# Optimization experiments

Measured on AMD Instinct MI355X. Metric: run time of the kernel, lower is better.

Reference implementation:

```python
import jax, jax.numpy as jnp
import numpy as np

SEQ, D_IN, D_OUT = 4096, 1024, 1024


def setup_inputs() -> dict:
    key = jax.random.key(0)
    k_emb, k_q, k_k, k_v = jax.random.split(key, 4)
    # torch Linear stores weight as [out, in]; we keep [in, out] for x @ W
    scale = 1.0 / np.sqrt(D_IN)
    return {
        "embeddings": jax.random.normal(k_emb, (SEQ, D_IN), dtype=jnp.float32),
        "w_query": jax.random.uniform(k_q, (D_IN, D_OUT), dtype=jnp.float32, minval=-scale, maxval=scale),
        "w_key": jax.random.uniform(k_k, (D_IN, D_OUT), dtype=jnp.float32, minval=-scale, maxval=scale),
        "w_value": jax.random.uniform(k_v, (D_IN, D_OUT), dtype=jnp.float32, minval=-scale, maxval=scale),
    }


def reference(embeddings, w_query, w_key, w_value):
    # QKV projections (bias=False)
    q = embeddings @ w_query  # [S, D_out]
    k = embeddings @ w_key    # [S, D_out]
    v = embeddings @ w_value  # [S, D_out]
    inv_sqrt_d = 1.0 / jnp.sqrt(jnp.asarray(k.shape[-1], dtype=q.dtype))
    scores = jnp.einsum("sd,td->st", q, k) * inv_sqrt_d  # [S, S]
    weights = jax.nn.softmax(scores, axis=-1)
    return weights @ v  # [S, D_out]
```

## Files before the change

kernel.cpp:

```cpp
#include <hip/hip_runtime.h>
#include <hip/hip_bf16.h>

typedef unsigned short u16;
typedef __bf16 bf16x8 __attribute__((ext_vector_type(8)));
typedef float f32x4 __attribute__((ext_vector_type(4)));
typedef unsigned short u16x8 __attribute__((ext_vector_type(8)));
typedef unsigned short u16x4 __attribute__((ext_vector_type(4)));

__device__ __forceinline__ float bf2f(u16 u) {
  unsigned x = ((unsigned)u) << 16;
  return __builtin_bit_cast(float, x);
}
__device__ __forceinline__ u16 f2bf(float f) {
  unsigned u = __builtin_bit_cast(unsigned, f);
  u += 0x7fffu + ((u >> 16) & 1u);
  return (u16)(u >> 16);
}

__device__ __forceinline__ void gload16(const u16* g, u16* lds) {
  __builtin_amdgcn_global_load_lds(
      (const __attribute__((address_space(1))) void*)g,
      (__attribute__((address_space(3))) void*)lds,
      16, 0, 0);
}

__device__ __forceinline__ void bar() {
  __builtin_amdgcn_sched_barrier(0);
  __builtin_amdgcn_s_barrier();
  __builtin_amdgcn_sched_barrier(0);
}
template <int N> __device__ __forceinline__ void wait_vm() {
  asm volatile("s_waitcnt vmcnt(%0)" :: "n"(N) : "memory");
  __builtin_amdgcn_sched_barrier(0);
}
__device__ __forceinline__ void wait_lgkm0() {
  asm volatile("s_waitcnt lgkmcnt(0)" ::: "memory");
  __builtin_amdgcn_sched_barrier(0);
}

#define OFF_A(d,h) (((d)*2+(h))*8192)
#define OFF_B(d,h) (32768 + ((d)*2+(h))*8192)

struct G256 {
  const u16 *gA0, *gA1, *gB0, *gB1;
  int dst0, dst1;
  int aoff0[4], aoff1[4], boff[4];
  u16* lds;
};

__device__ __forceinline__ int swz_slot(int row, int q) {
  return row * 4 + (q ^ ((row ^ (row >> 2)) & 3));
}

__device__ __forceinline__ void mfma_quad(f32x4 (*accr)[4], const bf16x8* af, const bf16x8* bf) {
#pragma unroll
  for (int i = 0; i < 4; ++i)
#pragma unroll
    for (int j = 0; j < 4; ++j)
      accr[i][j] = __builtin_amdgcn_mfma_f32_16x16x32_bf16(af[i], bf[j], accr[i][j], 0, 0, 0);
}

template <int W1, int W3, bool S01, bool S23>
__device__ __forceinline__ void ktile256(const G256& g, int s, f32x4 (&acc)[8][4]) {
  const int d = s & 1;
  bf16x8 af[4], bf[4];
  const int kA1 = (s + 1) * 64 + 32;
  const int kA0 = (s + 2) * 64;

#pragma unroll
  for (int i = 0; i < 4; ++i) af[i] = *(const bf16x8*)(g.lds + OFF_A(d, 0) + g.aoff0[i]);
#pragma unroll
  for (int j = 0; j < 4; ++j) bf[j] = *(const bf16x8*)(g.lds + OFF_B(d, 0) + g.boff[j]);
  if (S01) {
    gload16(g.gA0 + kA1, g.lds + OFF_A(d ^ 1, 1) + g.dst0);
    gload16(g.gA1 + kA1, g.lds + OFF_A(d ^ 1, 1) + g.dst1);
  }
  bar();
  wait_lgkm0();
  __builtin_amdgcn_s_setprio(1);
  mfma_quad(&acc[0], af, bf);
  __builtin_amdgcn_s_setprio(0);
  bar();

#pragma unroll
  for (int i = 0; i < 4; ++i) af[i] = *(const bf16x8*)(g.lds + OFF_A(d, 0) + g.aoff1[i]);
  if (S01) {
    gload16(g.gB0 + kA1, g.lds + OFF_B(d ^ 1, 1) + g.dst0);
    gload16(g.gB1 + kA1, g.lds + OFF_B(d ^ 1, 1) + g.dst1);
  }
  wait_vm<W1>();
  bar();
  wait_lgkm0();
  __builtin_amdgcn_s_setprio(1);
  mfma_quad(&acc[4], af, bf);
  __builtin_amdgcn_s_setprio(0);
  bar();

#pragma unroll
  for (int i = 0; i < 4; ++i) af[i] = *(const bf16x8*)(g.lds + OFF_A(d, 1) + g.aoff0[i]);
#pragma unroll
  for (int j = 0; j < 4; ++j) bf[j] = *(const bf16x8*)(g.lds + OFF_B(d, 1) + g.boff[j]);
  if (S23) {
    gload16(g.gA0 + kA0, g.lds + OFF_A(d, 0) + g.dst0);
    gload16(g.gA1 + kA0, g.lds + OFF_A(d, 0) + g.dst1);
  }
  bar();
  wait_lgkm0();
  __builtin_amdgcn_s_setprio(1);
  mfma_quad(&acc[0], af, bf);
  __builtin_amdgcn_s_setprio(0);
  bar();

#pragma unroll
  for (int i = 0; i < 4; ++i) af[i] = *(const bf16x8*)(g.lds + OFF_A(d, 1) + g.aoff1[i]);
  if (S23) {
    gload16(g.gB0 + kA0, g.lds + OFF_B(d, 0) + g.dst0);
    gload16(g.gB1 + kA0, g.lds + OFF_B(d, 0) + g.dst1);
  }
  if constexpr (W3 >= 0) wait_vm<(W3 >= 0 ? W3 : 0)>();
  bar();
  wait_lgkm0();
  __builtin_amdgcn_s_setprio(1);
  mfma_quad(&acc[4], af, bf);
  __builtin_amdgcn_s_setprio(0);
  bar();
}

template <int NX, int NT>
__device__ __forceinline__ void gemm256_body(
    const u16* __restrict__ A, int lda, const u16* __restrict__ B, int ldb,
    u16* __restrict__ C, int ldc, float cscale, u16* lds, int bid)
{
  static_assert(NT >= 3, "tail peel needs NT>=3");
  const int by = (bid & 7) + 8 * (bid / (8 * NX));
  const int bx = (bid >> 3) % NX;
  const int m0 = by * 256, n0 = bx * 256;
  const int t = threadIdx.x;
  const int w = t >> 6, l = t & 63;
  const int wm = (w >> 2) * 128, wn = (w & 3) * 64;
  const int fr = l & 15, q = l >> 4;

  G256 g;
  g.lds = lds;
  {
    const int s0 = w * 64 + l;
    const int r0 = s0 >> 2, r1 = r0 + 128;
    const int q0 = (s0 & 3) ^ ((r0 ^ (r0 >> 2)) & 3);
    const int q1 = (s0 & 3) ^ ((r1 ^ (r1 >> 2)) & 3);
    g.gA0 = A + (size_t)(m0 + r0) * lda + q0 * 8;
    g.gA1 = A + (size_t)(m0 + r1) * lda + q1 * 8;
    g.gB0 = B + (size_t)(n0 + r0) * ldb + q0 * 8;
    g.gB1 = B + (size_t)(n0 + r1) * ldb + q1 * 8;
    g.dst0 = (w * 64) * 8;
    g.dst1 = (512 + w * 64) * 8;
  }
#pragma unroll
  for (int i = 0; i < 4; ++i) {
    g.aoff0[i] = swz_slot(wm + 16 * i + fr, q) * 8;
    g.aoff1[i] = swz_slot(wm + 64 + 16 * i + fr, q) * 8;
    g.boff[i]  = swz_slot(wn + 16 * i + fr, q) * 8;
  }

  f32x4 acc[8][4] = {};

  gload16(g.gA0 + 0,  lds + OFF_A(0, 0) + g.dst0);
  gload16(g.gA1 + 0,  lds + OFF_A(0, 0) + g.dst1);
  gload16(g.gB0 + 0,  lds + OFF_B(0, 0) + g.dst0);
  gload16(g.gB1 + 0,  lds + OFF_B(0, 0) + g.dst1);
  gload16(g.gA0 + 32, lds + OFF_A(0, 1) + g.dst0);
  gload16(g.gA1 + 32, lds + OFF_A(0, 1) + g.dst1);
  gload16(g.gB0 + 32, lds + OFF_B(0, 1) + g.dst0);
  gload16(g.gB1 + 32, lds + OFF_B(0, 1) + g.dst1);
  gload16(g.gA0 + 64, lds + OFF_A(1, 0) + g.dst0);
  gload16(g.gA1 + 64, lds + OFF_A(1, 0) + g.dst1);
  gload16(g.gB0 + 64, lds + OFF_B(1, 0) + g.dst0);
  gload16(g.gB1 + 64, lds + OFF_B(1, 0) + g.dst1);
  wait_vm<8>();
  bar();

  for (int s = 0; s + 2 < NT; ++s)
    ktile256<8, 8, true, true>(g, s, acc);
  ktile256<8, 4, true, false>(g, NT - 2, acc);
  ktile256<0, -1, false, false>(g, NT - 1, acc);

  const int er = q * 4, ec = fr;
  const int rg = l >> 3, c = l & 7;
  u16* eb = lds + w * 4608;
#pragma unroll
  for (int half = 0; half < 2; ++half) {
#pragma unroll
    for (int i = 0; i < 4; ++i)
#pragma unroll
      for (int j = 0; j < 4; ++j)
#pragma unroll
        for (int r = 0; r < 4; ++r)
          eb[(16 * i + er + r) * 72 + 16 * j + ec] = f2bf(acc[4 * half + i][j][r] * cscale);
#pragma unroll
    for (int k = 0; k < 8; ++k) {
      const int row = k * 8 + rg;
      u16x8 v = *(const u16x8*)(eb + row * 72 + c * 8);
      *(u16x8*)(C + (size_t)(m0 + wm + 64 * half + row) * ldc + n0 + wn + c * 8) = v;
    }
  }
}

__global__ __launch_bounds__(512, 2) void gemm_qkv256(const u16* __restrict__ A,
                                                      const u16* __restrict__ B,
                                                      u16* __restrict__ C) {
  __shared__ __align__(16) u16 lds[65536];
  gemm256_body<12, 16>(A, 1024, B, 1024, C, 3072, 1.0f, lds, blockIdx.x);
}

__global__ __launch_bounds__(512, 2) void gemm_score256(const u16* __restrict__ QKV,
                                                        u16* __restrict__ S) {
  __shared__ __align__(16) u16 lds[65536];
  gemm256_body<16, 16>(QKV, 3072, QKV + 1024, 3072, S, 4096, 0.03125f, lds, blockIdx.x);
}

template <int OUT_MODE, int NX, int BK, int BN>
__device__ __forceinline__ void gemm_body(
    const u16* __restrict__ A, int lda,
    const u16* __restrict__ B, int ldb,
    void* __restrict__ C, int ldc, int kt0, int Kc, float cscale,
    u16* lds, int bid)
{
  u16* As = lds;
  u16* Bs = lds + 128 * BK;

  constexpr int CPR = BK / 8;
  constexpr int RPG = 512 / BK;
  constexpr int IPA = 32 / RPG;
  constexpr int IPB = (BN / 4) / RPG;
  constexpr int NWN = BN / 32;

  const int by = (bid & 7) + 8 * (bid / (8 * NX));
  const int bx = (bid >> 3) % NX;
  const int m0 = by * 128, n0 = bx * BN;

  const int t = threadIdx.x;
  const int w = t >> 6, l = t & 63;
  const int srow = l / CPR;
  const int lc = l % CPR;
  const int wm = (w >> 1) * 64;
  const int wn = (w & 1) * (BN / 2);
  const int fr = l & 15;
  const int q = l >> 4;

  f32x4 acc[4][NWN] = {};

  for (int kk = 0; kk < Kc; kk += BK) {
    const int kt = kt0 + kk;
    __syncthreads();
#pragma unroll
    for (int j = 0; j < IPA; ++j) {
      const int rr = RPG * (IPA * w + j);
      const int ga = rr + srow;
      const int sch = ((lc ^ (ga & 7))) * 8;
      gload16(A + (size_t)(m0 + ga) * lda + kt + sch, As + rr * BK);
    }
#pragma unroll
    for (int j = 0; j < IPB; ++j) {
      const int rr = RPG * (IPB * w + j);
      const int gb = rr + srow;
      const int sch = ((lc ^ (gb & 7))) * 8;
      gload16(B + (size_t)(n0 + gb) * ldb + kt + sch, Bs + rr * BK);
    }
    __syncthreads();

#pragma unroll
    for (int s = 0; s < BK / 32; ++s) {
      const int j = s * 4 + q;
      bf16x8 af[4], bfr[NWN];
#pragma unroll
      for (int i = 0; i < 4; ++i) {
        const int ra = wm + 16 * i + fr;
        af[i] = *(const bf16x8*)(As + ra * BK + (j ^ (ra & 7)) * 8);
      }
#pragma unroll
      for (int i = 0; i < NWN; ++i) {
        const int rb = wn + 16 * i + fr;
        bfr[i] = *(const bf16x8*)(Bs + rb * BK + (j ^ (rb & 7)) * 8);
      }
#pragma unroll
      for (int i = 0; i < 4; ++i)
#pragma unroll
        for (int jj = 0; jj < NWN; ++jj)
          acc[i][jj] = __builtin_amdgcn_mfma_f32_16x16x32_bf16(af[i], bfr[jj], acc[i][jj], 0, 0, 0);
    }
  }

  __syncthreads();
  const int er = q * 4;
  const int ec = l & 15;
  const int g = l >> 3, c = l & 7;

  if (OUT_MODE == 1) {
    u16* eb = lds + w * 4608;
#pragma unroll
    for (int i = 0; i < 4; ++i)
#pragma unroll
      for (int jj = 0; jj < NWN; ++jj)
#pragma unroll
        for (int r = 0; r < 4; ++r)
          eb[(16 * i + er + r) * 72 + 16 * jj + ec] = f2bf(acc[i][jj][r] * cscale);
#pragma unroll
    for (int k = 0; k < 8; ++k) {
      const int row = k * 8 + g;
      u16x8 v = *(const u16x8*)(eb + row * 72 + c * 8);
      *(u16x8*)((u16*)C + (size_t)(m0 + wm + row) * ldc + n0 + wn + c * 8) = v;
    }
  } else {
    float* eb = (float*)lds + w * 2560;
#pragma unroll
    for (int i = 0; i < 4; ++i)
#pragma unroll
      for (int jj = 0; jj < NWN; ++jj)
#pragma unroll
        for (int r = 0; r < 4; ++r)
          eb[(16 * i + er + r) * 40 + 16 * jj + ec] = acc[i][jj][r];
#pragma unroll
    for (int k = 0; k < 8; ++k) {
      const int row = k * 8 + g;
      float4 v = *(const float4*)(eb + row * 40 + c * 4);
      *(float4*)((float*)C + (size_t)(m0 + wm + row) * ldc + n0 + wn + c * 4) = v;
    }
  }
}

__global__ __launch_bounds__(256) void gemm_pv(const u16* __restrict__ S,
                                               const u16* __restrict__ Vt,
                                               float* __restrict__ O) {
  __shared__ __align__(16) u16 lds[24576];
  gemm_body<0, 16, 128, 64>(S, 4096, Vt, 4096, O, 1024, 0, 4096,
                            1.0f, lds, blockIdx.x);
}

__global__ __launch_bounds__(256) void prep(
    const float* __restrict__ E,
    const float* __restrict__ w0, const float* __restrict__ w1,
    const float* __restrict__ w2,
    u16* __restrict__ Ebf, u16* __restrict__ Wt)
{
  int b = blockIdx.x;
  if (b < 4096) {
    const int i = (b * 256 + threadIdx.x) * 4;
    float4 f = *(const float4*)(E + i);
    u16x4 o;
    o.x = f2bf(f.x); o.y = f2bf(f.y); o.z = f2bf(f.z); o.w = f2bf(f.w);
    *(u16x4*)(Ebf + i) = o;
  } else {
    b -= 4096;
    const int which = b >> 10;
    const int tile = b & 1023;
    const float* in = (which == 0) ? w0 : (which == 1) ? w1 : w2;
    u16* o = Wt + (size_t)which * 1024 * 1024;
    const int c0 = (tile & 31) * 32, r0 = (tile >> 5) * 32;
    __shared__ u16 tl[32][33];
    const int tx = threadIdx.x & 31, ty0 = threadIdx.x >> 5;
#pragma unroll
    for (int k = 0; k < 4; ++k) {
      const int ty = ty0 + k * 8;
      tl[ty][tx] = f2bf(in[(size_t)(r0 + ty) * 1024 + c0 + tx]);
    }
    __syncthreads();
#pragma unroll
    for (int k = 0; k < 4; ++k) {
      const int ty = ty0 + k * 8;
      o[(size_t)(c0 + ty) * 1024 + r0 + tx] = tl[tx][ty];
    }
  }
}

__global__ __launch_bounds__(256) void softmax_tv(u16* __restrict__ S,
                                                  const u16* __restrict__ QKV,
                                                  u16* __restrict__ Vt) {
  __shared__ float red[8];
  __shared__ u16 tl[32][33];
  const int b = blockIdx.x;
  if (b < 4096) {
    const int N = 4096;
    u16* p = S + (size_t)b * N;
    const int t = threadIdx.x;
    u16x8 u0 = ((const u16x8*)p)[t * 2];
    u16x8 u1 = ((const u16x8*)p)[t * 2 + 1];
    float v[16];
#pragma unroll
    for (int i = 0; i < 8; ++i) v[i] = bf2f(u0[i]);
#pragma unroll
    for (int i = 0; i < 8; ++i) v[8 + i] = bf2f(u1[i]);

    float m = -1e30f;
#pragma unroll
    for (int i = 0; i < 16; ++i) m = fmaxf(m, v[i]);
#pragma unroll
    for (int off = 32; off; off >>= 1) m = fmaxf(m, __shfl_xor(m, off));
    if ((t & 63) == 0) red[t >> 6] = m;
    __syncthreads();
    m = fmaxf(fmaxf(red[0], red[1]), fmaxf(red[2], red[3]));

    float s = 0.f;
#pragma unroll
    for (int i = 0; i < 16; ++i) { v[i] = __expf(v[i] - m); s += v[i]; }
#pragma unroll
    for (int off = 32; off; off >>= 1) s += __shfl_xor(s, off);
    if ((t & 63) == 0) red[4 + (t >> 6)] = s;
    __syncthreads();
    s = (red[4] + red[5]) + (red[6] + red[7]);
    const float inv = 1.0f / s;

    u16x8 o0, o1;
#pragma unroll
    for (int i = 0; i < 8; ++i) o0[i] = f2bf(v[i] * inv);
#pragma unroll
    for (int i = 0; i < 8; ++i) o1[i] = f2bf(v[8 + i] * inv);
    ((u16x8*)p)[t * 2] = o0;
    ((u16x8*)p)[t * 2 + 1] = o1;
  } else {
    const int v = b - 4096;
    const int c0 = (v & 31) * 32;
    const int r0 = (v >> 5) * 32;
    const int tx = threadIdx.x & 31, ty0 = threadIdx.x >> 5;
    const u16* Vin = QKV + 2048;
#pragma unroll
    for (int k = 0; k < 4; ++k) {
      const int ty = ty0 + k * 8;
      tl[ty][tx] = Vin[(size_t)(r0 + ty) * 3072 + c0 + tx];
    }
    __syncthreads();
#pragma unroll
    for (int k = 0; k < 4; ++k) {
      const int ty = ty0 + k * 8;
      Vt[(size_t)(c0 + ty) * 4096 + r0 + tx] = tl[tx][ty];
    }
  }
}

extern "C" void kernel_launch(void* const* d_in, const int* in_sizes, int n_in,
                              void* d_out, int out_size, void* d_ws, size_t ws_size,
                              hipStream_t stream) {
  const float* E  = (const float*)d_in[0];
  const float* Wq = (const float*)d_in[1];
  const float* Wk = (const float*)d_in[2];
  const float* Wv = (const float*)d_in[3];
  float* Out = (float*)d_out;

  char* w = (char*)d_ws;
  u16* Ebf = (u16*)(w);
  u16* Wt  = (u16*)(w + (size_t)(8u << 20));
  u16* QKV = (u16*)(w + (size_t)(14u << 20));
  u16* Vt  = (u16*)(w + (size_t)(38u << 20));
  u16* S   = (u16*)(w + (size_t)(46u << 20));

  prep<<<7168, 256, 0, stream>>>(E, Wq, Wk, Wv, Ebf, Wt);

  gemm_qkv256<<<192, 512, 0, stream>>>(Ebf, Wt, QKV);

  gemm_score256<<<256, 512, 0, stream>>>(QKV, S);

  softmax_tv<<<8192, 256, 0, stream>>>(S, QKV, Vt);

  gemm_pv<<<512, 256, 0, stream>>>(S, Vt, Out);
}
```

Before: 209.4 us.

## Split-K PV GEMM onto pipelined 256-tile kernel with partial-sum reduction

Replaces the simple 128-tile PV GEMM with the pipelined 256x256 GEMM body, using a 4-way split over the K (sequence) dimension so 256 workgroups run. Each split writes fp32 partials (or bf16 partials when the workspace is small) into a staging buffer, and a separate reduce kernel sums the four. This aims for better MFMA efficiency and occupancy on the PV product, at the cost of extra partial-buffer traffic and one more launch. The bf16 fallback also loses some precision.

```diff
diff --git a/kernel.cpp b/kernel.cpp
--- a/kernel.cpp
+++ b/kernel.cpp
@@ -126,10 +126,10 @@
   bar();
 }
 
-template <int NX, int NT>
+template <int OUT_MODE, int NX, int NT>
 __device__ __forceinline__ void gemm256_body(
     const u16* __restrict__ A, int lda, const u16* __restrict__ B, int ldb,
-    u16* __restrict__ C, int ldc, float cscale, u16* lds, int bid)
+    void* __restrict__ C, int ldc, float cscale, u16* lds, int bid)
 {
   static_assert(NT >= 3, "tail peel needs NT>=3");
   const int by = (bid & 7) + 8 * (bid / (8 * NX));
@@ -185,22 +185,50 @@
 
   const int er = q * 4, ec = fr;
   const int rg = l >> 3, c = l & 7;
-  u16* eb = lds + w * 4608;
-#pragma unroll
-  for (int half = 0; half < 2; ++half) {
-#pragma unroll
-    for (int i = 0; i < 4; ++i)
-#pragma unroll
-      for (int j = 0; j < 4; ++j)
-#pragma unroll
-        for (int r = 0; r < 4; ++r)
-          eb[(16 * i + er + r) * 72 + 16 * j + ec] = f2bf(acc[4 * half + i][j][r] * cscale);
-#pragma unroll
-    for (int k = 0; k < 8; ++k) {
-      const int row = k * 8 + rg;
-      u16x8 v = *(const u16x8*)(eb + row * 72 + c * 8);
-      *(u16x8*)(C + (size_t)(m0 + wm + 64 * half + row) * ldc + n0 + wn + c * 8) = v;
+
+  if (OUT_MODE == 1) {
+    u16* Ch = (u16*)C;
+    u16* eb = lds + w * 4608;
+#pragma unroll
+    for (int half = 0; half < 2; ++half) {
+#pragma unroll
+      for (int i = 0; i < 4; ++i)
+#pragma unroll
+        for (int j = 0; j < 4; ++j)
+#pragma unroll
+          for (int r = 0; r < 4; ++r)
+            eb[(16 * i + er + r) * 72 + 16 * j + ec] = f2bf(acc[4 * half + i][j][r] * cscale);
+#pragma unroll
+      for (int k = 0; k < 8; ++k) {
+        const int row = k * 8 + rg;
+        u16x8 v = *(const u16x8*)(eb + row * 72 + c * 8);
+        *(u16x8*)(Ch + (size_t)(m0 + wm + 64 * half + row) * ldc + n0 + wn + c * 8) = v;
+      }
     }
+  } else {
+    float* Cf = (float*)C;
+    float* eb = (float*)lds + w * 2304;
+#pragma unroll
+    for (int half = 0; half < 2; ++half)
+#pragma unroll
+      for (int ip = 0; ip < 2; ++ip) {
+#pragma unroll
+        for (int ii = 0; ii < 2; ++ii)
+#pragma unroll
+          for (int j = 0; j < 4; ++j)
+#pragma unroll
+            for (int r = 0; r < 4; ++r)
+              eb[(16 * ii + er + r) * 72 + 16 * j + ec] = acc[4 * half + 2 * ip + ii][j][r] * cscale;
+#pragma unroll
+        for (int k = 0; k < 4; ++k) {
+          const int row = k * 8 + rg;
+          float4 v0 = *(const float4*)(eb + row * 72 + c * 4);
+          float4 v1 = *(const float4*)(eb + row * 72 + (c + 8) * 4);
+          float* dst = Cf + (size_t)(m0 + wm + 64 * half + 32 * ip + row) * ldc + n0 + wn;
+          *(float4*)(dst + c * 4) = v0;
+          *(float4*)(dst + (c + 8) * 4) = v1;
+        }
+      }
   }
 }
 
@@ -208,131 +236,67 @@
                                                       const u16* __restrict__ B,
                                                       u16* __restrict__ C) {
   __shared__ __align__(16) u16 lds[65536];
-  gemm256_body<12, 16>(A, 1024, B, 1024, C, 3072, 1.0f, lds, blockIdx.x);
+  gemm256_body<1, 12, 16>(A, 1024, B, 1024, C, 3072, 1.0f, lds, blockIdx.x);
 }
 
 __global__ __launch_bounds__(512, 2) void gemm_score256(const u16* __restrict__ QKV,
                                                         u16* __restrict__ S) {
   __shared__ __align__(16) u16 lds[65536];
-  gemm256_body<16, 16>(QKV, 3072, QKV + 1024, 3072, S, 4096, 0.03125f, lds, blockIdx.x);
-}
-
-template <int OUT_MODE, int NX, int BK, int BN>
-__device__ __forceinline__ void gemm_body(
-    const u16* __restrict__ A, int lda,
-    const u16* __restrict__ B, int ldb,
-    void* __restrict__ C, int ldc, int kt0, int Kc, float cscale,
-    u16* lds, int bid)
-{
-  u16* As = lds;
-  u16* Bs = lds + 128 * BK;
-
-  constexpr int CPR = BK / 8;
-  constexpr int RPG = 512 / BK;
-  constexpr int IPA = 32 / RPG;
-  constexpr int IPB = (BN / 4) / RPG;
-  constexpr int NWN = BN / 32;
-
-  const int by = (bid & 7) + 8 * (bid / (8 * NX));
-  const int bx = (bid >> 3) % NX;
-  const int m0 = by * 128, n0 = bx * BN;
-
-  const int t = threadIdx.x;
-  const int w = t >> 6, l = t & 63;
-  const int srow = l / CPR;
-  const int lc = l % CPR;
-  const int wm = (w >> 1) * 64;
-  const int wn = (w & 1) * (BN / 2);
-  const int fr = l & 15;
-  const int q = l >> 4;
-
-  f32x4 acc[4][NWN] = {};
-
-  for (int kk = 0; kk < Kc; kk += BK) {
-    const int kt = kt0 + kk;
-    __syncthreads();
-#pragma unroll
-    for (int j = 0; j < IPA; ++j) {
-      const int rr = RPG * (IPA * w + j);
-      const int ga = rr + srow;
-      const int sch = ((lc ^ (ga & 7))) * 8;
-      gload16(A + (size_t)(m0 + ga) * lda + kt + sch, As + rr * BK);
-    }
-#pragma unroll
-    for (int j = 0; j < IPB; ++j) {
-      const int rr = RPG * (IPB * w + j);
-      const int gb = rr + srow;
-      const int sch = ((lc ^ (gb & 7))) * 8;
-      gload16(B + (size_t)(n0 + gb) * ldb + kt + sch, Bs + rr * BK);
-    }
-    __syncthreads();
-
-#pragma unroll
-    for (int s = 0; s < BK / 32; ++s) {
-      const int j = s * 4 + q;
-      bf16x8 af[4], bfr[NWN];
-#pragma unroll
-      for (int i = 0; i < 4; ++i) {
-        const int ra = wm + 16 * i + fr;
-        af[i] = *(const bf16x8*)(As + ra * BK + (j ^ (ra & 7)) * 8);
-      }
-#pragma unroll
-      for (int i = 0; i < NWN; ++i) {
-        const int rb = wn + 16 * i + fr;
-        bfr[i] = *(const bf16x8*)(Bs + rb * BK + (j ^ (rb & 7)) * 8);
-      }
-#pragma unroll
-      for (int i = 0; i < 4; ++i)
-#pragma unroll
-        for (int jj = 0; jj < NWN; ++jj)
-          acc[i][jj] = __builtin_amdgcn_mfma_f32_16x16x32_bf16(af[i], bfr[jj], acc[i][jj], 0, 0, 0);
-    }
-  }
-
-  __syncthreads();
-  const int er = q * 4;
-  const int ec = l & 15;
-  const int g = l >> 3, c = l & 7;
-
-  if (OUT_MODE == 1) {
-    u16* eb = lds + w * 4608;
-#pragma unroll
-    for (int i = 0; i < 4; ++i)
-#pragma unroll
-      for (int jj = 0; jj < NWN; ++jj)
-#pragma unroll
-        for (int r = 0; r < 4; ++r)
-          eb[(16 * i + er + r) * 72 + 16 * jj + ec] = f2bf(acc[i][jj][r] * cscale);
-#pragma unroll
-    for (int k = 0; k < 8; ++k) {
-      const int row = k * 8 + g;
-      u16x8 v = *(const u16x8*)(eb + row * 72 + c * 8);
-      *(u16x8*)((u16*)C + (size_t)(m0 + wm + row) * ldc + n0 + wn + c * 8) = v;
-    }
-  } else {
-    float* eb = (float*)lds + w * 2560;
-#pragma unroll
-    for (int i = 0; i < 4; ++i)
-#pragma unroll
-      for (int jj = 0; jj < NWN; ++jj)
-#pragma unroll
-        for (int r = 0; r < 4; ++r)
-          eb[(16 * i + er + r) * 40 + 16 * jj + ec] = acc[i][jj][r];
-#pragma unroll
-    for (int k = 0; k < 8; ++k) {
-      const int row = k * 8 + g;
-      float4 v = *(const float4*)(eb + row * 40 + c * 4);
-      *(float4*)((float*)C + (size_t)(m0 + wm + row) * ldc + n0 + wn + c * 4) = v;
-    }
-  }
-}
-
-__global__ __launch_bounds__(256) void gemm_pv(const u16* __restrict__ S,
-                                               const u16* __restrict__ Vt,
-                                               float* __restrict__ O) {
-  __shared__ __align__(16) u16 lds[24576];
-  gemm_body<0, 16, 128, 64>(S, 4096, Vt, 4096, O, 1024, 0, 4096,
-                            1.0f, lds, blockIdx.x);
+  gemm256_body<1, 16, 16>(QKV, 3072, QKV + 1024, 3072, S, 4096, 0.03125f, lds, blockIdx.x);
+}
+
+__global__ __launch_bounds__(512, 2) void gemm_pv256f(const u16* __restrict__ S,
+                                                      const u16* __restrict__ Vt,
+                                                      float* __restrict__ P4) {
+  __shared__ __align__(16) u16 lds[65536];
+  const int b = blockIdx.x;
+  const int sp = b >> 6;
+  float* Cp = P4 + (size_t)sp * 4096 * 1024;
+  gemm256_body<0, 4, 16>(S + sp * 1024, 4096, Vt + sp * 1024, 4096,
+                         Cp, 1024, 1.0f, lds, b & 63);
+}
+
+__global__ __launch_bounds__(512, 2) void gemm_pv256h(const u16* __restrict__ S,
+                                                      const u16* __restrict__ Vt,
+                                                      u16* __restrict__ P4) {
+  __shared__ __align__(16) u16 lds[65536];
+  const int b = blockIdx.x;
+  const int sp = b >> 6;
+  u16* Cp = P4 + (size_t)sp * 4096 * 1024;
+  gemm256_body<1, 4, 16>(S + sp * 1024, 4096, Vt + sp * 1024, 4096,
+                         Cp, 1024, 1.0f, lds, b & 63);
+}
+
+__global__ __launch_bounds__(256) void reduce4f(const float* __restrict__ P4,
+                                                float* __restrict__ O) {
+  const size_t i = ((size_t)blockIdx.x * 256 + threadIdx.x) * 4;
+  const size_t st = (size_t)4096 * 1024;
+  float4 a = *(const float4*)(P4 + i);
+  float4 b = *(const float4*)(P4 + st + i);
+  float4 c = *(const float4*)(P4 + 2 * st + i);
+  float4 d = *(const float4*)(P4 + 3 * st + i);
+  float4 o;
+  o.x = (a.x + b.x) + (c.x + d.x);
+  o.y = (a.y + b.y) + (c.y + d.y);
+  o.z = (a.z + b.z) + (c.z + d.z);
+  o.w = (a.w + b.w) + (c.w + d.w);
+  *(float4*)(O + i) = o;
+}
+
+__global__ __launch_bounds__(256) void reduce4h(const u16* __restrict__ P4,
+                                                float* __restrict__ O) {
+  const size_t i = ((size_t)blockIdx.x * 256 + threadIdx.x) * 4;
+  const size_t st = (size_t)4096 * 1024;
+  u16x4 a = *(const u16x4*)(P4 + i);
+  u16x4 b = *(const u16x4*)(P4 + st + i);
+  u16x4 c = *(const u16x4*)(P4 + 2 * st + i);
+  u16x4 d = *(const u16x4*)(P4 + 3 * st + i);
+  float4 o;
+  o.x = (bf2f(a.x) + bf2f(b.x)) + (bf2f(c.x) + bf2f(d.x));
+  o.y = (bf2f(a.y) + bf2f(b.y)) + (bf2f(c.y) + bf2f(d.y));
+  o.z = (bf2f(a.z) + bf2f(b.z)) + (bf2f(c.z) + bf2f(d.z));
+  o.w = (bf2f(a.w) + bf2f(b.w)) + (bf2f(c.w) + bf2f(d.w));
+  *(float4*)(O + i) = o;
 }
 
 __global__ __launch_bounds__(256) void prep(
@@ -459,5 +423,13 @@
 
   softmax_tv<<<8192, 256, 0, stream>>>(S, QKV, Vt);
 
-  gemm_pv<<<512, 256, 0, stream>>>(S, Vt, Out);
-}
+  if (ws_size >= ((size_t)146u << 20)) {
+    float* P4 = (float*)(w + ((size_t)78u << 20));
+    gemm_pv256f<<<256, 512, 0, stream>>>(S, Vt, P4);
+    reduce4f<<<4096, 256, 0, stream>>>(P4, Out);
+  } else {
+    u16* P4 = (u16*)w;
+    gemm_pv256h<<<256, 512, 0, stream>>>(S, Vt, P4);
+    reduce4h<<<4096, 256, 0, stream>>>(P4, Out);
+  }
+}
```

Result: slower. 215.9 us (+3.1%).
